# Optimization experiments

Measured on AMD Instinct MI355X. Metric: run time of the kernel, lower is better.

Reference implementation:

```python
import jax, jax.numpy as jnp
import numpy as np
from jax import lax

S = 3000      # number of stocks (and number of targets)
F = 6         # raw features
N = 128       # hidden size
L = 40        # lookback length
L_MAX = 10    # max lag
K = 5         # topk leaders


def setup_inputs() -> dict:
    key = jax.random.key(0)
    ks = jax.random.split(key, 16)
    sc = 1.0 / np.sqrt(N)
    u = lambda k, shp, s=sc: jax.random.uniform(k, shp, jnp.float32, -s, s)
    return {
        "X_scaled": jax.random.normal(ks[0], (1, S, L, F), jnp.float32),
        "X_raw": jax.random.normal(ks[1], (1, S, L, F), jnp.float32),
        "target_idx": jax.random.randint(ks[2], (S,), 0, S, jnp.int32),
        "lstm_Wih": u(ks[3], (4 * N, F)),
        "lstm_Whh": u(ks[4], (4 * N, N)),
        "lstm_bih": u(ks[5], (4 * N,)),
        "lstm_bhh": u(ks[6], (4 * N,)),
        "ln_g": jnp.ones((N,), jnp.float32),
        "ln_b": jnp.zeros((N,), jnp.float32),
        "WQ": u(ks[7], (N, N)),
        "WK": u(ks[8], (N, N)),
        "log_temp": jnp.asarray(np.log(N ** 0.25), jnp.float32),
        "lag_bias": jnp.zeros((L_MAX,), jnp.float32),
        "W1": u(ks[9], (64, 2 * F), 1.0 / np.sqrt(2 * F)),
        "b1": jnp.zeros((64,), jnp.float32),
        "W2": u(ks[10], (32, 64), 1.0 / 8.0),
        "b2": jnp.zeros((32,), jnp.float32),
        "W3": u(ks[11], (1, 32), 1.0 / np.sqrt(32)),
        "b3": jnp.zeros((1,), jnp.float32),
    }


def _lstm(x, Wih, Whh, bih, bhh):
    # x: [BS, L, F] -> hidden sequence [BS, L, N]; torch gate order i,f,g,o
    BS = x.shape[0]
    h0 = jnp.zeros((BS, N), x.dtype)
    bias = bih + bhh

    def step(carry, xt):
        h, c = carry
        g = xt @ Wih.T + h @ Whh.T + bias
        i, f, gg, o = jnp.split(g, 4, axis=-1)
        c = jax.nn.sigmoid(f) * c + jax.nn.sigmoid(i) * jnp.tanh(gg)
        h = jax.nn.sigmoid(o) * jnp.tanh(c)
        return (h, c), h

    _, hs = lax.scan(step, (h0, h0), jnp.swapaxes(x, 0, 1))
    return jnp.swapaxes(hs, 0, 1)


def _ln(x, g, b):
    m = x.mean(-1, keepdims=True)
    v = ((x - m) ** 2).mean(-1, keepdims=True)
    return (x - m) / jnp.sqrt(v + 1e-5) * g + b


def _l2norm(x):
    return x / jnp.clip(jnp.linalg.norm(x, axis=-1, keepdims=True), 1e-12)


def reference(X_scaled, X_raw, target_idx, lstm_Wih, lstm_Whh, lstm_bih,
              lstm_bhh, ln_g, ln_b, WQ, WK, log_temp, lag_bias,
              W1, b1, W2, b2, W3, b3):
    # TemporalEncoder: LSTM over B*S sequences + LayerNorm (B=1)
    H = _ln(_lstm(X_scaled.reshape(S, L, F), lstm_Wih, lstm_Whh,
                  lstm_bih, lstm_bhh), ln_g, ln_b)          # [S, L, N]
    X = X_raw[0]                                            # [S, L, F]

    q = _l2norm(H[target_idx, -1] @ WQ.T)                   # [T, N]
    Hk = _l2norm(H[:, L - L_MAX:] @ WK.T)                   # [S, l_max, N]
    temp = jnp.clip(jnp.exp(log_temp), 0.1, N ** 0.5)

    attn = jnp.einsum('tn,sln->tsl', q, Hk) / temp + lag_bias  # [T, S, l_max]
    self_mask = jnp.arange(S)[None, :] == target_idx[:, None]  # [T, S]
    attn = jnp.where(self_mask[:, :, None], -jnp.inf, attn)

    vals, idx = lax.top_k(attn.reshape(-1, S * L_MAX), K)   # [T, K]
    leader = idx // L_MAX
    lag_j = idx % L_MAX
    lag_pos = jnp.clip(L - 1 - (L_MAX - lag_j), 0, L - 1)

    z = X[leader, lag_pos]                                  # [T, K, F]
    w = jax.nn.softmax(vals, axis=1)
    z_agg = (w[..., None] * z).sum(1)                       # [T, F]
    feat = jnp.concatenate([z_agg, z[:, 0]], axis=-1)       # [T, 2F]

    h1 = jax.nn.relu(feat @ W1.T + b1)
    h2 = jax.nn.relu(h1 @ W2.T + b2)
    return (h2 @ W3.T + b3).squeeze(-1)                     # [T]
```

## Files before the change

### kernel.cpp

```cpp
#include <hip/hip_runtime.h>
#include <math.h>

#define S_N 3000
#define NCOLS 30000
#define SCHUNK 8
#define KTILES 938
#define TPC 118
#define PST 17

typedef __bf16 v8bf __attribute__((ext_vector_type(8)));
typedef float v16f __attribute__((ext_vector_type(16)));
typedef float v4f __attribute__((ext_vector_type(4)));

__device__ __forceinline__ float sigm(float x) { return 1.0f / (1.0f + expf(-x)); }

__device__ __forceinline__ bool bet(float av, int ai, float bv, int bi) {
  return (av > bv) || (av == bv && ai < bi);
}

template <int M>
__device__ __forceinline__ void insS(float (&v)[M], int (&ix)[M], float nv, int ni) {
  if (!(nv > v[M - 1])) return;
  bool b[M];
#pragma unroll
  for (int q = 0; q < M; q++) b[q] = nv > v[q];
#pragma unroll
  for (int q = M - 1; q > 0; q--) {
    v[q]  = b[q] ? (b[q - 1] ? v[q - 1] : nv) : v[q];
    ix[q] = b[q] ? (b[q - 1] ? ix[q - 1] : ni) : ix[q];
  }
  if (b[0]) { v[0] = nv; ix[0] = ni; }
}

template <int M>
__device__ __forceinline__ void insF(float (&v)[M], int (&ix)[M], float nv, int ni) {
  if (!bet(nv, ni, v[M - 1], ix[M - 1])) return;
  bool b[M];
#pragma unroll
  for (int q = 0; q < M; q++) b[q] = bet(nv, ni, v[q], ix[q]);
#pragma unroll
  for (int q = M - 1; q > 0; q--) {
    v[q]  = b[q] ? (b[q - 1] ? v[q - 1] : nv) : v[q];
    ix[q] = b[q] ? (b[q - 1] ? ix[q - 1] : ni) : ix[q];
  }
  if (b[0]) { v[0] = nv; ix[0] = ni; }
}

__device__ __forceinline__ unsigned short f2bf_rne(float f) {
  unsigned int u = __float_as_uint(f);
  unsigned int r = (u + 0x7fffu + ((u >> 16) & 1u)) >> 16;
  return (unsigned short)r;
}
__device__ __forceinline__ float bf2f(unsigned short h) {
  return __uint_as_float(((unsigned int)h) << 16);
}

__global__ __launch_bounds__(256) void cvt_wll(
    const float* __restrict__ Whh, unsigned short* __restrict__ Wllf)
{
  int idx = blockIdx.x * 256 + threadIdx.x;
  if (idx >= 128 * 512) return;
  int f = idx >> 9;
  int lane = (idx >> 3) & 63;
  int j = idx & 7;
  int w = f >> 3, tau = (f >> 1) & 3, s = f & 1;
  int kh = w >> 3, g8 = w & 7;
  int gate = g8 * 64 + tau * 16 + (lane & 15);
  int k = kh * 64 + s * 32 + (lane >> 4) * 8 + j;
  float x = Whh[gate * 128 + k];
  unsigned short hi = f2bf_rne(x);
  float r1 = x - bf2f(hi);
  unsigned short lo = f2bf_rne(r1);
  float r2 = r1 - bf2f(lo);
  Wllf[idx] = f2bf_rne(r2);
}

__global__ __launch_bounds__(1024, 4) void lstm_kernel(
    const float* __restrict__ Xs, const float* __restrict__ Wih,
    const float* __restrict__ Whh, const float* __restrict__ bih,
    const float* __restrict__ bhh, const unsigned short* __restrict__ Wllf,
    float* __restrict__ H10)
{
  __shared__ float P[2 * 512 * PST];
  __shared__ __align__(16) __bf16 Asp[3][4][64][8];
  __shared__ float Xb[12 * 240];
  __shared__ float2 WB2[14][128];

  const int tid = threadIdx.x;
  const int s0 = blockIdx.x * 12;
  const int lane = tid & 63;
  const int wv = tid >> 6;
  const int kh = wv >> 3;
  const int g8 = wv & 7;
  const int l15 = lane & 15, lq = lane >> 4;

  for (int i = tid; i < 12 * 240; i += 1024) Xb[i] = Xs[(size_t)s0 * 240 + i];
  for (int i = tid; i < 3 * 4 * 64 * 8; i += 1024)
    ((unsigned short*)Asp)[i] = 0;
  for (int i = tid; i < 14 * 128; i += 1024) {
    int q = i >> 7, n = i & 127;
    float vv[2];
#pragma unroll
    for (int e = 0; e < 2; e++) {
      int r = 2 * q + e;
      if (r < 24) {
        int gate = n + (r / 6) * 128;
        vv[e] = Wih[gate * 6 + r % 6];
      } else {
        int gate = n + (r - 24) * 128;
        vv[e] = bih[gate] + bhh[gate];
      }
    }
    WB2[q][n] = make_float2(vv[0], vv[1]);
  }

  v8bf whi[4][2], wlo[4][2];
#pragma unroll
  for (int tau = 0; tau < 4; tau++)
#pragma unroll
    for (int s = 0; s < 2; s++) {
      int gate = g8 * 64 + tau * 16 + l15;
      int k0 = kh * 64 + s * 32 + lq * 8;
      const float* wp = Whh + gate * 128 + k0;
      v8bf h8, l8;
#pragma unroll
      for (int j = 0; j < 8; j++) {
        float x = wp[j];
        __bf16 bh_ = (__bf16)x;
        float r1 = x - (float)bh_;
        __bf16 bl_ = (__bf16)r1;
        h8[j] = bh_;
        l8[j] = bl_;
      }
      whi[tau][s] = h8;
      wlo[tau][s] = l8;
    }

  const unsigned short* wllbase = Wllf + (size_t)(wv * 8) * 512 + lane * 8;

  float c0 = 0.0f, c1 = 0.0f;
  const int p2n = tid & 127;
  const int p2m = tid >> 7;

  __syncthreads();

#pragma unroll 1
  for (int t = 0; t < 40; t++) {
    v8bf ah[2], al[2], a3[2];
#pragma unroll
    for (int s = 0; s < 2; s++) {
      int ks = kh * 2 + s;
      ah[s] = *(const v8bf*)&Asp[0][ks][lane][0];
      al[s] = *(const v8bf*)&Asp[1][ks][lane][0];
      a3[s] = *(const v8bf*)&Asp[2][ks][lane][0];
    }
#pragma unroll
    for (int tau = 0; tau < 4; tau++) {
      v4f acc = {0.0f, 0.0f, 0.0f, 0.0f};
#pragma unroll
      for (int s = 0; s < 2; s++) {
        v8bf wll = *(const v8bf*)(wllbase + (tau * 2 + s) * 512);
        acc = __builtin_amdgcn_mfma_f32_16x16x32_bf16(ah[s], whi[tau][s], acc, 0, 0, 0);
        acc = __builtin_amdgcn_mfma_f32_16x16x32_bf16(ah[s], wlo[tau][s], acc, 0, 0, 0);
        acc = __builtin_amdgcn_mfma_f32_16x16x32_bf16(al[s], whi[tau][s], acc, 0, 0, 0);
        acc = __builtin_amdgcn_mfma_f32_16x16x32_bf16(al[s], wlo[tau][s], acc, 0, 0, 0);
        acc = __builtin_amdgcn_mfma_f32_16x16x32_bf16(ah[s], wll, acc, 0, 0, 0);
        acc = __builtin_amdgcn_mfma_f32_16x16x32_bf16(a3[s], whi[tau][s], acc, 0, 0, 0);
      }
      if (lq < 3) {
        int gate = g8 * 64 + tau * 16 + l15;
        float* pp = P + kh * (512 * PST) + gate * PST + lq * 4;
#pragma unroll
        for (int reg = 0; reg < 4; reg++) pp[reg] = acc[reg];
      }
    }
    __syncthreads();

#pragma unroll
    for (int task = 0; task < 2; task++) {
      if (task == 1 && tid >= 512) break;
      const int m = task == 0 ? p2m : 8 + p2m;
      const int n = p2n;
      float wb[28];
#pragma unroll
      for (int q = 0; q < 14; q++) {
        float2 v = WB2[q][n];
        wb[2 * q] = v.x;
        wb[2 * q + 1] = v.y;
      }
      const float* xm = Xb + m * 240 + t * 6;
      float xv[6];
#pragma unroll
      for (int f = 0; f < 6; f++) xv[f] = xm[f];
      float g4[4];
#pragma unroll
      for (int g = 0; g < 4; g++) {
        float a = wb[24 + g];
#pragma unroll
        for (int f = 0; f < 6; f++) a = fmaf(wb[g * 6 + f], xv[f], a);
        int gate = n + g * 128;
        a += P[gate * PST + m] + P[512 * PST + gate * PST + m];
        g4[g] = a;
      }
      float& c = task == 0 ? c0 : c1;
      c = sigm(g4[1]) * c + sigm(g4[0]) * tanhf(g4[2]);
      float h = sigm(g4[3]) * tanhf(c);
      if (t >= 30) H10[((size_t)(s0 + m) * 10 + (t - 30)) * 128 + n] = h;
      __bf16 hh = (__bf16)h;
      float r1 = h - (float)hh;
      __bf16 hl = (__bf16)r1;
      float r2 = r1 - (float)hl;
      __bf16 h3 = (__bf16)r2;
      int ks = n >> 5, li = m + 16 * ((n >> 3) & 3), j = n & 7;
      Asp[0][ks][li][j] = hh;
      Asp[1][ks][li][j] = hl;
      Asp[2][ks][li][j] = h3;
    }
    __syncthreads();
  }
}

__global__ __launch_bounds__(256) void ln_kernel(
    float* __restrict__ H, const float* __restrict__ g,
    const float* __restrict__ b, int nrows)
{
  int row = blockIdx.x * 4 + (threadIdx.x >> 6);
  int lane = threadIdx.x & 63;
  if (row >= nrows) return;
  float* hr = H + (size_t)row * 128;
  float x0 = hr[lane], x1 = hr[lane + 64];
  float s = x0 + x1;
  for (int off = 32; off > 0; off >>= 1) s += __shfl_xor(s, off);
  float mean = s * (1.0f / 128.0f);
  float d0 = x0 - mean, d1 = x1 - mean;
  float v = d0 * d0 + d1 * d1;
  for (int off = 32; off > 0; off >>= 1) v += __shfl_xor(v, off);
  float rstd = 1.0f / sqrtf(v * (1.0f / 128.0f) + 1e-5f);
  hr[lane] = d0 * rstd * g[lane] + b[lane];
  hr[lane + 64] = d1 * rstd * g[lane + 64] + b[lane + 64];
}

__global__ __launch_bounds__(256) void proj_kernel(
    const float* __restrict__ In, int inOff, int inStride, int nr,
    const float* __restrict__ W, float* __restrict__ Out)
{
  __shared__ float A_s[16 * 128];
  const int tid = threadIdx.x;
  const int r0 = blockIdx.x * 16;

  for (int i = tid; i < 16 * 32; i += 256) {
    int row = i >> 5, c = i & 31;
    int gr = r0 + row;
    float4 v = make_float4(0.f, 0.f, 0.f, 0.f);
    if (gr < nr)
      v = *(const float4*)(In + (size_t)inOff + (size_t)gr * inStride + c * 4);
    *(float4*)(A_s + row * 128 + c * 4) = v;
  }
  __syncthreads();

  const int j = tid & 127, rh = tid >> 7;
  const float* wrow = W + j * 128;
  float acc[8] = {0, 0, 0, 0, 0, 0, 0, 0};
  for (int kc = 0; kc < 32; kc++) {
    float4 wv4 = *(const float4*)(wrow + kc * 4);
#pragma unroll
    for (int i = 0; i < 8; i++) {
      float4 a4 = *(const float4*)(A_s + (rh * 8 + i) * 128 + kc * 4);
      acc[i] = fmaf(wv4.x, a4.x, acc[i]);
      acc[i] = fmaf(wv4.y, a4.y, acc[i]);
      acc[i] = fmaf(wv4.z, a4.z, acc[i]);
      acc[i] = fmaf(wv4.w, a4.w, acc[i]);
    }
  }
  __syncthreads();
#pragma unroll
  for (int i = 0; i < 8; i++) A_s[(rh * 8 + i) * 128 + j] = acc[i];
  __syncthreads();

  const int r = tid >> 4, qq = tid & 15;
  float ss = 0.0f;
#pragma unroll
  for (int i = 0; i < 8; i++) {
    float u = A_s[r * 128 + qq + i * 16];
    ss += u * u;
  }
  for (int off = 8; off > 0; off >>= 1) ss += __shfl_xor(ss, off);
  float scale = 1.0f / fmaxf(sqrtf(ss), 1e-12f);
  int gr = r0 + r;
  if (gr < nr) {
#pragma unroll
    for (int i = 0; i < 8; i++)
      Out[(size_t)gr * 128 + qq + i * 16] = A_s[r * 128 + qq + i * 16] * scale;
  }
}

__global__ __launch_bounds__(256) void cvt_kernel(
    const float* __restrict__ src, unsigned short* __restrict__ hi,
    unsigned short* __restrict__ lo, int n4)
{
  int i = blockIdx.x * 256 + threadIdx.x;
  if (i >= n4) return;
  float4 f = ((const float4*)src)[i];
  ushort4 h, l;
  h.x = f2bf_rne(f.x); l.x = f2bf_rne(f.x - bf2f(h.x));
  h.y = f2bf_rne(f.y); l.y = f2bf_rne(f.y - bf2f(h.y));
  h.z = f2bf_rne(f.z); l.z = f2bf_rne(f.z - bf2f(h.z));
  h.w = f2bf_rne(f.w); l.w = f2bf_rne(f.w - bf2f(h.w));
  ((ushort4*)hi)[i] = h;
  ((ushort4*)lo)[i] = l;
}

__global__ __launch_bounds__(256) void cvt_blockK(
    const float* __restrict__ Kn, unsigned short* __restrict__ hi,
    unsigned short* __restrict__ lo)
{
  const int tile = blockIdx.x;
  const int tid = threadIdx.x;
#pragma unroll
  for (int jj = 0; jj < 4; jj++) {
    int i = tid + jj * 256;
    int r = i >> 5;
    int c0 = (i & 31) * 4;
    int row = tile * 32 + r;
    if (row >= NCOLS) continue;
    float4 f = *(const float4*)(Kn + (size_t)row * 128 + c0);
    ushort4 h, l;
    h.x = f2bf_rne(f.x); l.x = f2bf_rne(f.x - bf2f(h.x));
    h.y = f2bf_rne(f.y); l.y = f2bf_rne(f.y - bf2f(h.y));
    h.z = f2bf_rne(f.z); l.z = f2bf_rne(f.z - bf2f(h.z));
    h.w = f2bf_rne(f.w); l.w = f2bf_rne(f.w - bf2f(h.w));
    int s = c0 >> 4, half = (c0 >> 3) & 1, e = c0 & 7;
    size_t idx = (size_t)tile * 4096 + s * 512 + half * 256 + r * 8 + e;
    *(ushort4*)(hi + idx) = h;
    *(ushort4*)(lo + idx) = l;
  }
}

__global__ __launch_bounds__(256, 3) void score_mfma(
    const unsigned short* __restrict__ Qh, const unsigned short* __restrict__ Ql,
    const unsigned short* __restrict__ Kh, const unsigned short* __restrict__ Kl,
    const int* __restrict__ tix, const float* __restrict__ log_temp,
    const float* __restrict__ lag_bias, float* __restrict__ part)
{
  __shared__ float lagS2[42];
  __shared__ float M[256 * 16];
  const int tid = threadIdx.x;
  const int wv = tid >> 6, lane = tid & 63;
  const int half = lane >> 5, tcol = lane & 31;

  const int lid = blockIdx.y * 94 + blockIdx.x;
  const int chunk = lid & 7;
  const int T0 = (lid >> 3) * 32;
  const int tstart = chunk * TPC;
  const int tend = (tstart + TPC < KTILES) ? tstart + TPC : KTILES;

  for (int i = tid; i < 42; i += 256) lagS2[i] = lag_bias[i % 10];

  const int tgt = T0 + tcol;
  const int tgtc = tgt < S_N ? tgt : S_N - 1;
  const int myTix = tix[tgtc];
  const int selfLo = myTix * 10;
  const float invtemp =
      1.0f / fminf(fmaxf(expf(log_temp[0]), 0.1f), 11.313708499f);

  v8bf bh[8], bl[8];
  {
    const size_t qo = (size_t)myTix * 128 + half * 8;
#pragma unroll
    for (int s = 0; s < 8; s++) {
      bh[s] = *(const v8bf*)(Qh + qo + s * 16);
      bl[s] = *(const v8bf*)(Ql + qo + s * 16);
    }
  }
#pragma unroll
  for (int s = 0; s < 8; s++) {
    asm volatile("" : "+v"(bh[s]), "+v"(bl[s]));
  }

  float tv[8]; int ti[8];
#pragma unroll
  for (int q = 0; q < 8; q++) { tv[q] = -3e38f; ti[q] = 0x7fffffff; }

  __syncthreads();

  for (int it = 0; it < 30; it++) {
    const int tile = tstart + it * 4 + wv;
    const int tilec = tile < KTILES ? tile : KTILES - 1;
    const size_t ao = (size_t)tilec * 4096 + half * 256 + tcol * 8;

    v16f acc0, acc1;
#pragma unroll
    for (int q = 0; q < 16; q++) { acc0[q] = 0.0f; acc1[q] = 0.0f; }

#pragma unroll
    for (int s = 0; s < 8; s++) {
      v8bf ah = *(const v8bf*)(Kh + ao + s * 512);
      v8bf al = *(const v8bf*)(Kl + ao + s * 512);
      acc0 = __builtin_amdgcn_mfma_f32_32x32x16_bf16(ah, bh[s], acc0, 0, 0, 0);
      acc1 = __builtin_amdgcn_mfma_f32_32x32x16_bf16(ah, bl[s], acc1, 0, 0, 0);
      acc1 = __builtin_amdgcn_mfma_f32_32x32x16_bf16(al, bh[s], acc1, 0, 0, 0);
    }

    const int cb = tile * 32;
    const int m0 = cb % 10;
    const bool act = tile < tend;
#pragma unroll
    for (int reg = 0; reg < 16; reg++) {
      const int row = (reg & 3) + 8 * (reg >> 2) + 4 * half;
      const int col = cb + row;
      float vsc = fmaf(acc0[reg] + acc1[reg], invtemp, lagS2[m0 + row]);
      if (act && col < NCOLS && (unsigned)(col - selfLo) >= 10u)
        insS<8>(tv, ti, vsc, col);
    }
  }

  {
    float* my = M + tid * 16;
#pragma unroll
    for (int q = 0; q < 8; q++) {
      my[2 * q] = tv[q];
      my[2 * q + 1] = __int_as_float(ti[q]);
    }
  }
  __syncthreads();
  if (tid < 32 && T0 + tid < S_N) {
    float v[8]; int ix[8];
#pragma unroll
    for (int q = 0; q < 8; q++) { v[q] = -3e38f; ix[q] = 0x7fffffff; }
    for (int w = 0; w < 8; w++) {
      const float* src = M + (w * 32 + tid) * 16;
#pragma unroll
      for (int q = 0; q < 8; q++)
        insF<8>(v, ix, src[2 * q], __float_as_int(src[2 * q + 1]));
    }
    float* dst = part + ((size_t)(T0 + tid) * SCHUNK + chunk) * 16;
#pragma unroll
    for (int q = 0; q < 8; q++) {
      dst[2 * q] = v[q];
      dst[2 * q + 1] = __int_as_float(ix[q]);
    }
  }
}

__global__ __launch_bounds__(256) void final_kernel(
    const float* __restrict__ part, const float* __restrict__ Qn,
    const float* __restrict__ Kn, const int* __restrict__ tix,
    const float* __restrict__ log_temp, const float* __restrict__ lag_bias,
    const float* __restrict__ Xraw,
    const float* __restrict__ W1, const float* __restrict__ b1,
    const float* __restrict__ W2, const float* __restrict__ b2,
    const float* __restrict__ W3, const float* __restrict__ b3,
    float* __restrict__ out)
{
  __shared__ float W1s[64 * 12];
  __shared__ float W2s[32 * 64];
  __shared__ float b1s[64];
  __shared__ float b2s[32];
  __shared__ float W3s[32];
  const int tid = threadIdx.x;
  for (int i = tid; i < 768; i += 256) W1s[i] = W1[i];
  for (int i = tid; i < 2048; i += 256) W2s[i] = W2[i];
  if (tid < 64) b1s[tid] = b1[tid];
  if (tid < 32) { b2s[tid] = b2[tid]; W3s[tid] = W3[tid]; }
  __syncthreads();

  int t = blockIdx.x * 256 + tid;
  if (t >= S_N) return;

  float av[8]; int ai[8];
#pragma unroll
  for (int q = 0; q < 8; q++) { av[q] = -3e38f; ai[q] = 0x7fffffff; }
  const float* pp = part + (size_t)t * (SCHUNK * 16);
  for (int c = 0; c < SCHUNK * 8; c++)
    insF<8>(av, ai, pp[2 * c], __float_as_int(pp[2 * c + 1]));

  const float invtemp =
      1.0f / fminf(fmaxf(expf(log_temp[0]), 0.1f), 11.313708499f);
  const float* q = Qn + (size_t)tix[t] * 128;
  const float* kr[8];
#pragma unroll
  for (int j = 0; j < 8; j++) kr[j] = Kn + (size_t)ai[j] * 128;
  float d[8] = {0, 0, 0, 0, 0, 0, 0, 0};
  for (int kc = 0; kc < 32; kc++) {
    float4 q4 = ((const float4*)q)[kc];
#pragma unroll
    for (int j = 0; j < 8; j++) {
      float4 k4 = ((const float4*)kr[j])[kc];
      d[j] = fmaf(q4.x, k4.x, d[j]);
      d[j] = fmaf(q4.y, k4.y, d[j]);
      d[j] = fmaf(q4.z, k4.z, d[j]);
      d[j] = fmaf(q4.w, k4.w, d[j]);
    }
  }

  float v[5]; int ix[5];
#pragma unroll
  for (int qq = 0; qq < 5; qq++) { v[qq] = -3e38f; ix[qq] = 0x7fffffff; }
#pragma unroll
  for (int j = 0; j < 8; j++) {
    int c = ai[j];
    int s = c / 10;
    int lag = c - 10 * s;
    float ev = d[j] * invtemp + lag_bias[lag];
    insF<5>(v, ix, ev, c);
  }

  float e1 = expf(v[1] - v[0]), e2 = expf(v[2] - v[0]),
        e3 = expf(v[3] - v[0]), e4 = expf(v[4] - v[0]);
  float rs = 1.0f / (1.0f + e1 + e2 + e3 + e4);
  float w_[5] = {rs, e1 * rs, e2 * rs, e3 * rs, e4 * rs};

  float feat[12];
#pragma unroll
  for (int f = 0; f < 12; f++) feat[f] = 0.0f;
#pragma unroll
  for (int qq = 0; qq < 5; qq++) {
    int iq = ix[qq];
    int s = iq / 10;
    int l = iq - 10 * s;
    int pos = 29 + l;
    const float* zp = Xraw + (size_t)s * 240 + pos * 6;
#pragma unroll
    for (int f = 0; f < 6; f++) {
      float z = zp[f];
      feat[f] += w_[qq] * z;
      if (qq == 0) feat[6 + f] = z;
    }
  }

  float h1[64];
#pragma unroll 4
  for (int o = 0; o < 64; o++) {
    float acc = b1s[o];
    const float* wr = W1s + o * 12;
#pragma unroll
    for (int f = 0; f < 12; f++) acc = fmaf(wr[f], feat[f], acc);
    h1[o] = fmaxf(acc, 0.0f);
  }
  float rr = b3[0];
#pragma unroll 2
  for (int o = 0; o < 32; o++) {
    float acc = b2s[o];
    const float* wr = W2s + o * 64;
#pragma unroll 8
    for (int k = 0; k < 64; k++) acc = fmaf(wr[k], h1[k], acc);
    rr = fmaf(W3s[o], fmaxf(acc, 0.0f), rr);
  }
  out[t] = rr;
}

extern "C" void kernel_launch(void* const* d_in, const int* in_sizes, int n_in,
                              void* d_out, int out_size, void* d_ws,
                              size_t ws_size, hipStream_t stream) {
  const float* Xs   = (const float*)d_in[0];
  const float* Xraw = (const float*)d_in[1];
  const int*   tix  = (const int*)d_in[2];
  const float* Wih  = (const float*)d_in[3];
  const float* Whh  = (const float*)d_in[4];
  const float* bih  = (const float*)d_in[5];
  const float* bhh  = (const float*)d_in[6];
  const float* ln_g = (const float*)d_in[7];
  const float* ln_b = (const float*)d_in[8];
  const float* WQ   = (const float*)d_in[9];
  const float* WK   = (const float*)d_in[10];
  const float* log_temp = (const float*)d_in[11];
  const float* lag_bias = (const float*)d_in[12];
  const float* W1 = (const float*)d_in[13];
  const float* b1 = (const float*)d_in[14];
  const float* W2 = (const float*)d_in[15];
  const float* b2 = (const float*)d_in[16];
  const float* W3 = (const float*)d_in[17];
  const float* b3 = (const float*)d_in[18];
  float* outp = (float*)d_out;

  float* ws = (float*)d_ws;
  float* H10 = ws;
  unsigned short* Khi = (unsigned short*)ws;
  unsigned short* Klo = (unsigned short*)(ws + 1922000);
  float* Kn  = ws + 3850000;
  float* Qn  = ws + 7690000;
  unsigned short* Qhi = (unsigned short*)(ws + 8074000);
  unsigned short* Qlo = (unsigned short*)(ws + 8266000);
  float* part = ws + 8458000;
  unsigned short* Wllf = (unsigned short*)(ws + 9226000);

  cvt_wll<<<256, 256, 0, stream>>>(Whh, Wllf);
  lstm_kernel<<<250, 1024, 0, stream>>>(Xs, Wih, Whh, bih, bhh, Wllf, H10);
  ln_kernel<<<7500, 256, 0, stream>>>(H10, ln_g, ln_b, 30000);
  proj_kernel<<<1875, 256, 0, stream>>>(H10, 0, 128, 30000, WK, Kn);
  proj_kernel<<<188, 256, 0, stream>>>(H10, 9 * 128, 1280, 3000, WQ, Qn);
  cvt_blockK<<<KTILES, 256, 0, stream>>>(Kn, Khi, Klo);
  cvt_kernel<<<375, 256, 0, stream>>>(Qn, Qhi, Qlo, 96000);
  {
    dim3 grid(94, SCHUNK);
    score_mfma<<<grid, 256, 0, stream>>>(Qhi, Qlo, Khi, Klo, tix, log_temp,
                                         lag_bias, part);
  }
  final_kernel<<<12, 256, 0, stream>>>(part, Qn, Kn, tix, log_temp, lag_bias,
                                       Xraw, W1, b1, W2, b2, W3, b3, outp);
}
```

Baseline: 691.8 us.

## Fuse layernorm and bf16 split into projection; swizzle and pack LSTM LDS writes

Layernorm moves into proj_kernel, applied to the rows staged in shared memory, and the Q projection now writes its hi/lo bf16 split directly. This drops the separate ln_kernel and cvt_kernel launches and one full read-modify-write pass over the hidden states. In the LSTM kernel the hidden-state shared buffer gets an extra padding row and an XOR swizzle on rows. Adjacent lanes exchange values with shuffles so each even lane writes packed 32-bit words, which is meant to cut LDS bank conflicts and store count. The input-weight values are now read from shared memory per gate instead of held in a 28-float register array, easing register pressure at the cost of more LDS reads.

```diff
diff --git a/kernel.cpp b/kernel.cpp
--- a/kernel.cpp
+++ b/kernel.cpp
@@ -82,7 +82,7 @@
     float* __restrict__ H10)
 {
   __shared__ float P[2 * 512 * PST];
-  __shared__ __align__(16) __bf16 Asp[3][4][64][8];
+  __shared__ __align__(16) __bf16 Asp[3][4][65][8];
   __shared__ float Xb[12 * 240];
   __shared__ float2 WB2[14][128];
 
@@ -95,7 +95,7 @@
   const int l15 = lane & 15, lq = lane >> 4;
 
   for (int i = tid; i < 12 * 240; i += 1024) Xb[i] = Xs[(size_t)s0 * 240 + i];
-  for (int i = tid; i < 3 * 4 * 64 * 8; i += 1024)
+  for (int i = tid; i < 3 * 4 * 65 * 8; i += 1024)
     ((unsigned short*)Asp)[i] = 0;
   for (int i = tid; i < 14 * 128; i += 1024) {
     int q = i >> 7, n = i & 127;
@@ -141,6 +141,7 @@
   float c0 = 0.0f, c1 = 0.0f;
   const int p2n = tid & 127;
   const int p2m = tid >> 7;
+  const int swl = lane ^ (((lane >> 4) & 3) << 2);
 
   __syncthreads();
 
@@ -150,9 +151,9 @@
 #pragma unroll
     for (int s = 0; s < 2; s++) {
       int ks = kh * 2 + s;
-      ah[s] = *(const v8bf*)&Asp[0][ks][lane][0];
-      al[s] = *(const v8bf*)&Asp[1][ks][lane][0];
-      a3[s] = *(const v8bf*)&Asp[2][ks][lane][0];
+      ah[s] = *(const v8bf*)&Asp[0][ks][swl][0];
+      al[s] = *(const v8bf*)&Asp[1][ks][swl][0];
+      a3[s] = *(const v8bf*)&Asp[2][ks][swl][0];
     }
 #pragma unroll
     for (int tau = 0; tau < 4; tau++) {
@@ -181,13 +182,6 @@
       if (task == 1 && tid >= 512) break;
       const int m = task == 0 ? p2m : 8 + p2m;
       const int n = p2n;
-      float wb[28];
-#pragma unroll
-      for (int q = 0; q < 14; q++) {
-        float2 v = WB2[q][n];
-        wb[2 * q] = v.x;
-        wb[2 * q + 1] = v.y;
-      }
       const float* xm = Xb + m * 240 + t * 6;
       float xv[6];
 #pragma unroll
@@ -195,9 +189,17 @@
       float g4[4];
 #pragma unroll
       for (int g = 0; g < 4; g++) {
-        float a = wb[24 + g];
-#pragma unroll
-        for (int f = 0; f < 6; f++) a = fmaf(wb[g * 6 + f], xv[f], a);
+        float2 w01 = WB2[3 * g][n];
+        float2 w23 = WB2[3 * g + 1][n];
+        float2 w45 = WB2[3 * g + 2][n];
+        float2 bb = WB2[12 + (g >> 1)][n];
+        float a = (g & 1) ? bb.y : bb.x;
+        a = fmaf(w01.x, xv[0], a);
+        a = fmaf(w01.y, xv[1], a);
+        a = fmaf(w23.x, xv[2], a);
+        a = fmaf(w23.y, xv[3], a);
+        a = fmaf(w45.x, xv[4], a);
+        a = fmaf(w45.y, xv[5], a);
         int gate = n + g * 128;
         a += P[gate * PST + m] + P[512 * PST + gate * PST + m];
         g4[g] = a;
@@ -211,38 +213,33 @@
       __bf16 hl = (__bf16)r1;
       float r2 = r1 - (float)hl;
       __bf16 h3 = (__bf16)r2;
-      int ks = n >> 5, li = m + 16 * ((n >> 3) & 3), j = n & 7;
-      Asp[0][ks][li][j] = hh;
-      Asp[1][ks][li][j] = hl;
-      Asp[2][ks][li][j] = h3;
+      unsigned a01 = (unsigned)__builtin_bit_cast(unsigned short, hh) |
+                     ((unsigned)__builtin_bit_cast(unsigned short, hl) << 16);
+      unsigned a2 = (unsigned)__builtin_bit_cast(unsigned short, h3);
+      unsigned b01 = (unsigned)__shfl_xor((int)a01, 1);
+      unsigned b2 = (unsigned)__shfl_xor((int)a2, 1);
+      if (!(lane & 1)) {
+        int g = (n >> 3) & 3;
+        int ks = n >> 5;
+        int row = (m + 16 * g) ^ (g << 2);
+        int j0 = n & 7;
+        unsigned w0 = (a01 & 0xffffu) | (b01 << 16);
+        unsigned w1 = (a01 >> 16) | (b01 & 0xffff0000u);
+        unsigned w2 = a2 | (b2 << 16);
+        *(unsigned*)&Asp[0][ks][row][j0] = w0;
+        *(unsigned*)&Asp[1][ks][row][j0] = w1;
+        *(unsigned*)&Asp[2][ks][row][j0] = w2;
+      }
     }
     __syncthreads();
   }
-}
-
-__global__ __launch_bounds__(256) void ln_kernel(
-    float* __restrict__ H, const float* __restrict__ g,
-    const float* __restrict__ b, int nrows)
-{
-  int row = blockIdx.x * 4 + (threadIdx.x >> 6);
-  int lane = threadIdx.x & 63;
-  if (row >= nrows) return;
-  float* hr = H + (size_t)row * 128;
-  float x0 = hr[lane], x1 = hr[lane + 64];
-  float s = x0 + x1;
-  for (int off = 32; off > 0; off >>= 1) s += __shfl_xor(s, off);
-  float mean = s * (1.0f / 128.0f);
-  float d0 = x0 - mean, d1 = x1 - mean;
-  float v = d0 * d0 + d1 * d1;
-  for (int off = 32; off > 0; off >>= 1) v += __shfl_xor(v, off);
-  float rstd = 1.0f / sqrtf(v * (1.0f / 128.0f) + 1e-5f);
-  hr[lane] = d0 * rstd * g[lane] + b[lane];
-  hr[lane + 64] = d1 * rstd * g[lane + 64] + b[lane + 64];
 }
 
 __global__ __launch_bounds__(256) void proj_kernel(
     const float* __restrict__ In, int inOff, int inStride, int nr,
-    const float* __restrict__ W, float* __restrict__ Out)
+    const float* __restrict__ W, const float* __restrict__ lng,
+    const float* __restrict__ lnb, float* __restrict__ Out,
+    unsigned short* __restrict__ OutHi, unsigned short* __restrict__ OutLo)
 {
   __shared__ float A_s[16 * 128];
   const int tid = threadIdx.x;
@@ -258,6 +255,27 @@
   }
   __syncthreads();
 
+  {
+    const int wvv = tid >> 6, lane = tid & 63;
+    const float g0 = lng[lane], g1 = lng[lane + 64];
+    const float bb0 = lnb[lane], bb1 = lnb[lane + 64];
+#pragma unroll
+    for (int p = 0; p < 4; p++) {
+      float* hr = A_s + (wvv * 4 + p) * 128;
+      float x0 = hr[lane], x1 = hr[lane + 64];
+      float s = x0 + x1;
+      for (int off = 32; off > 0; off >>= 1) s += __shfl_xor(s, off);
+      float mean = s * (1.0f / 128.0f);
+      float d0 = x0 - mean, d1 = x1 - mean;
+      float v = d0 * d0 + d1 * d1;
+      for (int off = 32; off > 0; off >>= 1) v += __shfl_xor(v, off);
+      float rstd = 1.0f / sqrtf(v * (1.0f / 128.0f) + 1e-5f);
+      hr[lane] = d0 * rstd * g0 + bb0;
+      hr[lane + 64] = d1 * rstd * g1 + bb1;
+    }
+  }
+  __syncthreads();
+
   const int j = tid & 127, rh = tid >> 7;
   const float* wrow = W + j * 128;
   float acc[8] = {0, 0, 0, 0, 0, 0, 0, 0};
@@ -289,25 +307,18 @@
   int gr = r0 + r;
   if (gr < nr) {
 #pragma unroll
-    for (int i = 0; i < 8; i++)
-      Out[(size_t)gr * 128 + qq + i * 16] = A_s[r * 128 + qq + i * 16] * scale;
-  }
-}
-
-__global__ __launch_bounds__(256) void cvt_kernel(
-    const float* __restrict__ src, unsigned short* __restrict__ hi,
-    unsigned short* __restrict__ lo, int n4)
-{
-  int i = blockIdx.x * 256 + threadIdx.x;
-  if (i >= n4) return;
-  float4 f = ((const float4*)src)[i];
-  ushort4 h, l;
-  h.x = f2bf_rne(f.x); l.x = f2bf_rne(f.x - bf2f(h.x));
-  h.y = f2bf_rne(f.y); l.y = f2bf_rne(f.y - bf2f(h.y));
-  h.z = f2bf_rne(f.z); l.z = f2bf_rne(f.z - bf2f(h.z));
-  h.w = f2bf_rne(f.w); l.w = f2bf_rne(f.w - bf2f(h.w));
-  ((ushort4*)hi)[i] = h;
-  ((ushort4*)lo)[i] = l;
+    for (int i = 0; i < 8; i++) {
+      float val = A_s[r * 128 + qq + i * 16] * scale;
+      int col = qq + i * 16;
+      Out[(size_t)gr * 128 + col] = val;
+      if (OutHi) {
+        unsigned short h = f2bf_rne(val);
+        unsigned short l = f2bf_rne(val - bf2f(h));
+        OutHi[(size_t)gr * 128 + col] = h;
+        OutLo[(size_t)gr * 128 + col] = l;
+      }
+    }
+  }
 }
 
 __global__ __launch_bounds__(256) void cvt_blockK(
@@ -586,11 +597,11 @@
 
   cvt_wll<<<256, 256, 0, stream>>>(Whh, Wllf);
   lstm_kernel<<<250, 1024, 0, stream>>>(Xs, Wih, Whh, bih, bhh, Wllf, H10);
-  ln_kernel<<<7500, 256, 0, stream>>>(H10, ln_g, ln_b, 30000);
-  proj_kernel<<<1875, 256, 0, stream>>>(H10, 0, 128, 30000, WK, Kn);
-  proj_kernel<<<188, 256, 0, stream>>>(H10, 9 * 128, 1280, 3000, WQ, Qn);
+  proj_kernel<<<1875, 256, 0, stream>>>(H10, 0, 128, 30000, WK, ln_g, ln_b,
+                                        Kn, nullptr, nullptr);
+  proj_kernel<<<188, 256, 0, stream>>>(H10, 9 * 128, 1280, 3000, WQ, ln_g,
+                                       ln_b, Qn, Qhi, Qlo);
   cvt_blockK<<<KTILES, 256, 0, stream>>>(Kn, Khi, Klo);
-  cvt_kernel<<<375, 256, 0, stream>>>(Qn, Qhi, Qlo, 96000);
   {
     dim3 grid(94, SCHUNK);
     score_mfma<<<grid, 256, 0, stream>>>(Qhi, Qlo, Khi, Klo, tix, log_temp,
```

Result: no change. 687.1 us (-0.7%).
